# Kernel tuning notes

Hardware: AMD Instinct MI355X
Metric: run time of the kernel (lower is better)

## Reference

```python
import jax, jax.numpy as jnp
import numpy as np

B, L = 2, 1024
D_MODEL = 1024
D_STATE = 16
K = 3            # conv kernel (odd so padding=(K-1)//2 preserves L)
EXPAND = 1       # module is only shape-consistent with d_inner == d_model
D_INNER = D_MODEL * EXPAND


def setup_inputs() -> dict:
    key = jax.random.key(0)
    ks = jax.random.split(key, 10)
    s = 0.02
    x = jax.random.normal(ks[0], (B, L, D_MODEL), dtype=jnp.float32)
    W_in = jax.random.normal(ks[1], (D_MODEL, 2 * D_INNER), dtype=jnp.float32) * s
    conv_w = jax.random.normal(ks[2], (D_INNER, 1, K), dtype=jnp.float32) * s  # depthwise OIH
    W_B = jax.random.normal(ks[3], (D_INNER, D_STATE), dtype=jnp.float32) * s
    W_C = jax.random.normal(ks[4], (D_INNER, D_STATE), dtype=jnp.float32) * s
    W_delta = jax.random.normal(ks[5], (D_INNER, D_MODEL), dtype=jnp.float32) * s
    delta_base = jax.random.normal(ks[6], (D_MODEL,), dtype=jnp.float32)
    W_tau = jax.random.normal(ks[7], (D_MODEL, D_MODEL), dtype=jnp.float32) * s
    A_log = jnp.tile(jnp.log(jnp.arange(1, D_STATE + 1, dtype=jnp.float32)), (D_MODEL, 1))
    W_out = jax.random.normal(ks[8], (D_INNER, D_MODEL), dtype=jnp.float32) * s
    return {"x": x, "W_in": W_in, "conv_w": conv_w, "W_B": W_B, "W_C": W_C,
            "W_delta": W_delta, "delta_base": delta_base, "W_tau": W_tau,
            "A_log": A_log, "W_out": W_out}


def _silu(v):
    return v * jax.nn.sigmoid(v)


def _mamba_fwd(x, W_in, conv_w, W_B, W_C, W_delta, delta_base, W_tau, A_log, W_out):
    residual = x
    z = x @ W_in                               # [B,L,2*D_INNER]
    val, gate = jnp.split(z, 2, axis=-1)
    # depthwise causal-ish conv1d (padding=(K-1)//2)
    v = jnp.transpose(val, (0, 2, 1))          # [B,C,L]
    v = jax.lax.conv_general_dilated(
        v, conv_w, window_strides=(1,), padding=[((K - 1) // 2, (K - 1) // 2)],
        dimension_numbers=("NCH", "OIH", "NCH"), feature_group_count=D_INNER)
    val = jnp.transpose(_silu(v), (0, 2, 1))   # [B,L,D_INNER]

    B_proj = val @ W_B                          # [B,L,N]
    C_proj = val @ W_C                          # [B,L,N]
    combined_delta = val @ W_delta + delta_base # [B,L,D_MODEL]
    Delta = jax.nn.softplus(combined_delta @ W_tau)  # [B,L,D]

    A = -jnp.exp(A_log)                         # [D,N]
    dA = Delta[..., None] * A                   # [B,L,D,N]
    A_bar = jnp.exp(dA)
    B_bar = jnp.expm1(dA) / (dA + 1e-6) * Delta[..., None] * B_proj[:, :, None, :]

    def step(h, inp):
        a_t, b_t, c_t, u_t = inp                # a/b:[B,D,N], c:[B,N], u:[B,D]
        h = a_t * h + b_t * u_t[..., None]
        y_t = jnp.sum(h * c_t[:, None, :], axis=-1)  # [B,D]
        return h, y_t

    h0 = jnp.zeros((x.shape[0], D_INNER, D_STATE), dtype=x.dtype)
    xs = (jnp.moveaxis(A_bar, 1, 0), jnp.moveaxis(B_bar, 1, 0),
          jnp.moveaxis(C_proj, 1, 0), jnp.moveaxis(val, 1, 0))
    _, ys = jax.lax.scan(step, h0, xs)          # ys: [L,B,D]
    y = jnp.moveaxis(ys, 0, 1)                  # [B,L,D]

    out = (y * _silu(gate)) @ W_out + residual  # [B,L,D_MODEL]
    return out


def reference(x, W_in, conv_w, W_B, W_C, W_delta, delta_base, W_tau, A_log, W_out):
    return _mamba_fwd(x, W_in, conv_w, W_B, W_C, W_delta, delta_base, W_tau, A_log, W_out)
```

## Files before the change

kernel.cpp:

```cpp
#include <hip/hip_runtime.h>
#include <math.h>

#define BB 2
#define LL 1024
#define DM 1024
#define DI 1024
#define DS 16
#define ROWS (BB * LL)
#define CH 16
#define NCH (LL / CH)
#define NP 1152
#define NF 1152

typedef unsigned short ushort_t;
typedef __attribute__((ext_vector_type(8))) short short8;
typedef __attribute__((ext_vector_type(4))) float f32x4;
typedef __attribute__((ext_vector_type(4))) float f4;
typedef __attribute__((ext_vector_type(4))) ushort_t us4;

static __device__ __forceinline__ float sp_f(float x) {
    return fmaxf(x, 0.f) + log1pf(expf(-fabsf(x)));
}
static __device__ __forceinline__ ushort_t f2bf(float f) {
    unsigned u = __float_as_uint(f);
    u += 0x7fffu + ((u >> 16) & 1u);
    return (ushort_t)(u >> 16);
}
static __device__ __forceinline__ float bf2f(ushort_t s) {
    return __uint_as_float(((unsigned)s) << 16);
}

#define SWZ(L) ((L) ^ ((((L) >> 7) & 7) << 4))

static __device__ __forceinline__ void gl_lds16(const void* g, void* l) {
    __builtin_amdgcn_global_load_lds(
        (const __attribute__((address_space(1))) unsigned int*)g,
        (__attribute__((address_space(3))) unsigned int*)l, 16, 0, 0);
}

template <int ACT, bool HAS_BIAS, bool HAS_RES, bool OUTBF, int PROJMODE>
__global__ __launch_bounds__(256) void gemm_bf_k(
    const ushort_t* __restrict__ A, const ushort_t* __restrict__ Bt,
    const float* __restrict__ bias, const float* __restrict__ res,
    void* __restrict__ Cout, float* __restrict__ BpO, float* __restrict__ CpO,
    int M, int N, int K, int ldc)
{
    __shared__ __align__(16) char lsa[2][8192];
    __shared__ __align__(16) char lsb[2][16384];

    const int tid = threadIdx.x;
    const int lane = tid & 63;
    const int w = tid >> 6;
    const int wr = w >> 1, wc = w & 1;

    int wg = blockIdx.y * gridDim.x + blockIdx.x;
    const int nwg = gridDim.x * gridDim.y;
    wg = (wg & 7) * (nwg >> 3) + (wg >> 3);
    const int bx = wg % gridDim.x, by = wg / gridDim.x;
    const int row0 = by * 64, col0 = bx * 128;

    const int rl = lane & 15, q = lane >> 4;

    const char* gA[2];
#pragma unroll
    for (int j = 0; j < 2; ++j) {
        int L = SWZ((w * 2 + j) * 1024 + lane * 16);
        gA[j] = (const char*)A + ((size_t)(row0 + (L >> 7)) * K) * 2 + (L & 127);
    }
    const char* gB[4];
#pragma unroll
    for (int j = 0; j < 4; ++j) {
        int L = SWZ((w * 4 + j) * 1024 + lane * 16);
        gB[j] = (const char*)Bt + ((size_t)(col0 + (L >> 7)) * K) * 2 + (L & 127);
    }

    int LA[2][2], LB[4][2];
#pragma unroll
    for (int m = 0; m < 2; ++m)
#pragma unroll
        for (int kk = 0; kk < 2; ++kk)
            LA[m][kk] = SWZ((wr * 32 + m * 16 + rl) * 128 + kk * 64 + q * 16);
#pragma unroll
    for (int n = 0; n < 4; ++n)
#pragma unroll
        for (int kk = 0; kk < 2; ++kk)
            LB[n][kk] = SWZ((wc * 64 + n * 16 + rl) * 128 + kk * 64 + q * 16);

    f32x4 acc[2][4] = {};
    const int NT = K >> 6;

#pragma unroll
    for (int j = 0; j < 2; ++j) gl_lds16(gA[j], &lsa[0][(w * 2 + j) * 1024]);
#pragma unroll
    for (int j = 0; j < 4; ++j) gl_lds16(gB[j], &lsb[0][(w * 4 + j) * 1024]);

    int cur = 0;
    for (int kt = 0; kt < NT; ++kt) {
        if (kt + 1 < NT) {
            const int kb = (kt + 1) * 128;
#pragma unroll
            for (int j = 0; j < 2; ++j)
                gl_lds16(gA[j] + kb, &lsa[cur ^ 1][(w * 2 + j) * 1024]);
#pragma unroll
            for (int j = 0; j < 4; ++j)
                gl_lds16(gB[j] + kb, &lsb[cur ^ 1][(w * 4 + j) * 1024]);
            asm volatile("s_waitcnt vmcnt(6)\n\ts_barrier" ::: "memory");
        } else {
            asm volatile("s_waitcnt vmcnt(0)\n\ts_barrier" ::: "memory");
        }
        short8 af[2][2], bfr[4][2];
#pragma unroll
        for (int m = 0; m < 2; ++m)
#pragma unroll
            for (int kk = 0; kk < 2; ++kk)
                af[m][kk] = *(const short8*)(&lsa[cur][LA[m][kk]]);
#pragma unroll
        for (int n = 0; n < 4; ++n)
#pragma unroll
            for (int kk = 0; kk < 2; ++kk)
                bfr[n][kk] = *(const short8*)(&lsb[cur][LB[n][kk]]);
#pragma unroll
        for (int kk = 0; kk < 2; ++kk)
#pragma unroll
            for (int m = 0; m < 2; ++m)
#pragma unroll
                for (int n = 0; n < 4; ++n)
                    acc[m][n] = __builtin_amdgcn_mfma_f32_16x16x32_bf16(
                        af[m][kk], bfr[n][kk], acc[m][n], 0, 0, 0);
        asm volatile("s_barrier" ::: "memory");
        cur ^= 1;
    }

    float bia[4];
#pragma unroll
    for (int n = 0; n < 4; ++n) {
        int c = col0 + wc * 64 + n * 16 + rl;
        bia[n] = (HAS_BIAS && c < DM) ? bias[c] : 0.f;
    }
#pragma unroll
    for (int m = 0; m < 2; ++m) {
#pragma unroll
        for (int n = 0; n < 4; ++n) {
            int c = col0 + wc * 64 + n * 16 + rl;
#pragma unroll
            for (int i = 0; i < 4; ++i) {
                int r = row0 + wr * 32 + m * 16 + q * 4 + i;
                float v = acc[m][n][i];
                if (PROJMODE == 1 && c >= DM) {
                    if (c < DM + DS)          BpO[(size_t)r * DS + (c - DM)] = v;
                    else if (c < DM + 2 * DS) CpO[(size_t)r * DS + (c - DM - DS)] = v;
                } else if (PROJMODE == 2 && c >= DM) {
                    if (c == DM) BpO[r] = v;
                } else {
                    v += bia[n];
                    if (ACT == 1) v = sp_f(v);
                    if (HAS_RES) v += res[(size_t)r * ldc + c];
                    if (OUTBF) ((ushort_t*)Cout)[(size_t)r * ldc + c] = f2bf(v);
                    else       ((float*)Cout)[(size_t)r * ldc + c] = v;
                }
            }
        }
    }
}

static __device__ __forceinline__ void tconv_body(
    const float* __restrict__ in, ushort_t* __restrict__ out,
    int K, int N, int n0, int k0, float (*t)[33], int tid)
{
    int lx = tid & 31, ly = tid >> 5;
#pragma unroll
    for (int i = 0; i < 32; i += 8)
        t[ly + i][lx] = in[(size_t)(k0 + ly + i) * N + n0 + lx];
    __syncthreads();
#pragma unroll
    for (int i = 0; i < 32; i += 8)
        out[(size_t)(n0 + ly + i) * K + k0 + lx] = f2bf(t[lx][ly + i]);
}

__global__ __launch_bounds__(256) void prep_k(
    const float* __restrict__ x, const float* __restrict__ W_in,
    const float* __restrict__ W_B, const float* __restrict__ W_C,
    const float* __restrict__ W_delta, const float* __restrict__ db,
    const float* __restrict__ W_tau, const float* __restrict__ W_out,
    ushort_t* __restrict__ x_bf, ushort_t* __restrict__ WinT,
    ushort_t* __restrict__ WtT, ushort_t* __restrict__ WoT,
    ushort_t* __restrict__ WdX, ushort_t* __restrict__ WdcT)
{
    __shared__ float t[32][33];
    const int blk = blockIdx.x;
    const int tid = threadIdx.x;
    if (blk < 2048) {
        int i = blk * 256 + tid;
        f4 v = ((const f4*)x)[i];
        us4 o; o.x = f2bf(v.x); o.y = f2bf(v.y); o.z = f2bf(v.z); o.w = f2bf(v.w);
        ((us4*)x_bf)[i] = o;
    } else if (blk < 3072) {
        int i = (blk - 2048) * 256 + tid;
        f4 v = ((const f4*)W_delta)[i];
        us4 o; o.x = f2bf(v.x); o.y = f2bf(v.y); o.z = f2bf(v.z); o.w = f2bf(v.w);
        ((us4*)WdX)[i] = o;
    } else if (blk < 3584) {
        int i = (blk - 3072) * 256 + tid;
        int k = i & 1023, r = i >> 10;
        WdX[(size_t)(1024 + r) * 1024 + k] = (r == 0) ? f2bf(db[k]) : (ushort_t)0;
    } else if (blk < 5632) {
        int tau = blk - 3584;
        tconv_body(W_in, WinT, 1024, 2048, (tau & 63) * 32, (tau >> 6) * 32, t, tid);
    } else if (blk < 6656) {
        int tau = blk - 5632;
        tconv_body(W_tau, WtT, 1024, 1024, (tau & 31) * 32, (tau >> 5) * 32, t, tid);
    } else if (blk < 7680) {
        int tau = blk - 6656;
        tconv_body(W_out, WoT, 1024, 1024, (tau & 31) * 32, (tau >> 5) * 32, t, tid);
    } else {
        int i = (blk - 7680) * 256 + tid;
        int k = i & 1023, r = i >> 10;
        ushort_t v = 0;
        if (r < DS)          v = f2bf(W_B[(size_t)k * DS + r]);
        else if (r < 2 * DS) v = f2bf(W_C[(size_t)k * DS + (r - DS)]);
        WdcT[(size_t)(1024 + r) * 1024 + k] = v;
    }
}

__global__ __launch_bounds__(256) void conv_silu_k(
    const ushort_t* __restrict__ z_bf, const float* __restrict__ cw,
    ushort_t* __restrict__ val_bf)
{
    int t = blockIdx.x * 256 + threadIdx.x;
    int c0 = (t & 255) * 4;
    int row = t >> 8;
    int l = row & (LL - 1);
    const ushort_t* zr = z_bf + (size_t)row * (2 * DI) + c0;
    us4 zz = {0, 0, 0, 0};
    us4 vm = (l > 0)      ? *(const us4*)(zr - 2 * DI) : zz;
    us4 v0 = *(const us4*)(zr);
    us4 vp = (l < LL - 1) ? *(const us4*)(zr + 2 * DI) : zz;
    const f4* wp = (const f4*)(cw + (size_t)c0 * 3);
    f4 w0 = wp[0], w1 = wp[1], w2 = wp[2];
    float w[12];
#pragma unroll
    for (int k = 0; k < 4; ++k) { w[k] = w0[k]; w[4 + k] = w1[k]; w[8 + k] = w2[k]; }
    us4 o;
#pragma unroll
    for (int j = 0; j < 4; ++j) {
        float s = bf2f(vm[j]) * w[3 * j] + bf2f(v0[j]) * w[3 * j + 1]
                + bf2f(vp[j]) * w[3 * j + 2];
        float si = s / (1.f + __expf(-s));
        o[j] = f2bf(si);
    }
    *(us4*)(val_bf + (size_t)row * DI + c0) = o;
}

__global__ __launch_bounds__(256) void scan_p1_k(
    const ushort_t* __restrict__ Del_bf, const ushort_t* __restrict__ val_bf,
    const float* __restrict__ Bp, const float* __restrict__ A_log,
    float* __restrict__ aprod, float* __restrict__ hloc)
{
    int t = blockIdx.x * 256 + threadIdx.x;
    int d = t & (DI - 1);
    int c = (t >> 10) & (NCH - 1);
    int b = t >> 16;

    float Adn[DS], ci[DS];
    const f4* alp = (const f4*)(A_log + (size_t)d * DS);
#pragma unroll
    for (int j = 0; j < 4; ++j) {
        f4 al = alp[j];
#pragma unroll
        for (int k = 0; k < 4; ++k) {
            float a = -__expf(al[k]);
            Adn[j * 4 + k] = a;
            ci[j * 4 + k] = 1.0f / a;
        }
    }
    int row0 = b * LL + c * CH;
    const ushort_t* Dp = Del_bf + (size_t)row0 * DI + d;
    const ushort_t* up = val_bf + (size_t)row0 * DI + d;
    const f4* bp = (const f4*)(Bp + (size_t)row0 * DS);

    float h[DS];
#pragma unroll
    for (int n = 0; n < DS; ++n) h[n] = 0.f;
    float sdv = 0.f;

#pragma unroll 2
    for (int l = 0; l < CH; ++l) {
        float dv = bf2f(Dp[(size_t)l * DI]);
        float u  = bf2f(up[(size_t)l * DI]);
        f4 q0 = bp[l * 4 + 0], q1 = bp[l * 4 + 1], q2 = bp[l * 4 + 2], q3 = bp[l * 4 + 3];
        float bn[DS];
#pragma unroll
        for (int k = 0; k < 4; ++k) {
            bn[k] = q0[k]; bn[4 + k] = q1[k]; bn[8 + k] = q2[k]; bn[12 + k] = q3[k];
        }
        sdv += dv;
#pragma unroll
        for (int n = 0; n < DS; ++n) {
            float a  = __expf(dv * Adn[n]);
            float tt = (ci[n] * bn[n]) * u;
            float s  = h[n] + tt;
            h[n] = fmaf(a, s, -tt);
        }
    }
    size_t o = (((size_t)b * NCH + c) * DI + d) * DS;
#pragma unroll
    for (int j = 0; j < 4; ++j) {
        f4 hv, av;
#pragma unroll
        for (int k = 0; k < 4; ++k) {
            hv[k] = h[j * 4 + k];
            av[k] = __expf(sdv * Adn[j * 4 + k]);
        }
        *(f4*)(hloc + o + j * 4) = hv;
        *(f4*)(aprod + o + j * 4) = av;
    }
}

__global__ __launch_bounds__(256) void scan_p2_k(
    const float* __restrict__ aprod, const float* __restrict__ hloc,
    float* __restrict__ hin)
{
    int t = blockIdx.x * 256 + threadIdx.x;
    int dn = t & (DI * DS - 1);
    int b = t >> 14;
    float h = 0.f;
    size_t base = (size_t)b * NCH * DI * DS + dn;
#pragma unroll 4
    for (int c = 0; c < NCH; ++c) {
        size_t idx = base + (size_t)c * (DI * DS);
        hin[idx] = h;
        h = fmaf(aprod[idx], h, hloc[idx]);
    }
}

__global__ __launch_bounds__(256) void scan_p3_k(
    const ushort_t* __restrict__ Del_bf, const ushort_t* __restrict__ val_bf,
    const float* __restrict__ Bp, const float* __restrict__ Cp,
    const float* __restrict__ A_log, const float* __restrict__ hin,
    const ushort_t* __restrict__ z_bf, ushort_t* __restrict__ g_bf)
{
    int t = blockIdx.x * 256 + threadIdx.x;
    int d = t & (DI - 1);
    int c = (t >> 10) & (NCH - 1);
    int b = t >> 16;

    float Adn[DS], ci[DS];
    const f4* alp = (const f4*)(A_log + (size_t)d * DS);
#pragma unroll
    for (int j = 0; j < 4; ++j) {
        f4 al = alp[j];
#pragma unroll
        for (int k = 0; k < 4; ++k) {
            float a = -__expf(al[k]);
            Adn[j * 4 + k] = a;
            ci[j * 4 + k] = 1.0f / a;
        }
    }
    int row0 = b * LL + c * CH;
    const ushort_t* Dp = Del_bf + (size_t)row0 * DI + d;
    const ushort_t* up = val_bf + (size_t)row0 * DI + d;
    const ushort_t* zp = z_bf + (size_t)row0 * (2 * DI) + DI + d;
    const f4* bp = (const f4*)(Bp + (size_t)row0 * DS);
    const f4* cp = (const f4*)(Cp + (size_t)row0 * DS);
    ushort_t* gp = g_bf + (size_t)row0 * DI + d;

    float h[DS];
    size_t o = (((size_t)b * NCH + c) * DI + d) * DS;
#pragma unroll
    for (int j = 0; j < 4; ++j) {
        f4 hv = *(const f4*)(hin + o + j * 4);
#pragma unroll
        for (int k = 0; k < 4; ++k) h[j * 4 + k] = hv[k];
    }

#pragma unroll 2
    for (int l = 0; l < CH; ++l) {
        float dv = bf2f(Dp[(size_t)l * DI]);
        float u  = bf2f(up[(size_t)l * DI]);
        f4 q0 = bp[l * 4 + 0], q1 = bp[l * 4 + 1], q2 = bp[l * 4 + 2], q3 = bp[l * 4 + 3];
        f4 r0 = cp[l * 4 + 0], r1 = cp[l * 4 + 1], r2 = cp[l * 4 + 2], r3 = cp[l * 4 + 3];
        float bn[DS], cn[DS];
#pragma unroll
        for (int k = 0; k < 4; ++k) {
            bn[k] = q0[k]; bn[4 + k] = q1[k]; bn[8 + k] = q2[k]; bn[12 + k] = q3[k];
            cn[k] = r0[k]; cn[4 + k] = r1[k]; cn[8 + k] = r2[k]; cn[12 + k] = r3[k];
        }
        float psum = 0.f;
#pragma unroll
        for (int n = 0; n < DS; ++n) {
            float a  = __expf(dv * Adn[n]);
            float tt = (ci[n] * bn[n]) * u;
            float s  = h[n] + tt;
            h[n] = fmaf(a, s, -tt);
            psum = fmaf(h[n], cn[n], psum);
        }
        float zg = bf2f(zp[(size_t)l * 2 * DI]);
        float si = zg / (1.f + __expf(-zg));
        gp[(size_t)l * DI] = f2bf(psum * si);
    }
}

extern "C" void kernel_launch(void* const* d_in, const int* in_sizes, int n_in,
                              void* d_out, int out_size, void* d_ws, size_t ws_size,
                              hipStream_t stream)
{
    (void)in_sizes; (void)n_in; (void)out_size; (void)ws_size;

    const float* x        = (const float*)d_in[0];
    const float* W_in     = (const float*)d_in[1];
    const float* conv_w   = (const float*)d_in[2];
    const float* W_B      = (const float*)d_in[3];
    const float* W_C      = (const float*)d_in[4];
    const float* W_delta  = (const float*)d_in[5];
    const float* delta_b  = (const float*)d_in[6];
    const float* W_tau    = (const float*)d_in[7];
    const float* A_log    = (const float*)d_in[8];
    const float* W_out    = (const float*)d_in[9];
    float* out = (float*)d_out;

    const size_t M1 = 1024 * 1024;
    ushort_t* us = (ushort_t*)d_ws;
    ushort_t* z_bf   = us;
    ushort_t* val_bf = us + 4 * M1;
    ushort_t* Del_bf = us + 6 * M1;
    ushort_t* x_bf   = us + 8 * M1;
    ushort_t* g_bf   = us + 10 * M1;
    ushort_t* WinT   = us + 12 * M1;
    ushort_t* WoT    = us + 14 * M1;
    ushort_t* WtT    = us + 15 * M1;
    ushort_t* WdX    = us + 16 * M1;
    ushort_t* WdcT   = WdX + (size_t)NF * 1024;
    float* fb    = (float*)(us + 20 * M1);
    float* Bp    = fb;
    float* Cp    = fb + (size_t)ROWS * DS;
    float* b2    = fb + 2 * (size_t)ROWS * DS;
    float* aprod = b2 + 1024;
    float* hloc  = aprod + 2 * M1;
    float* hin   = hloc + 2 * M1;

    prep_k<<<8192, 256, 0, stream>>>(x, W_in, W_B, W_C, W_delta, delta_b,
                                     W_tau, W_out, x_bf, WinT, WtT, WoT, WdX, WdcT);

    gemm_bf_k<0, false, false, true, 2><<<dim3(NF / 128, DM / 64), 256, 0, stream>>>(
        WtT, WdX, nullptr, nullptr, WdcT, b2, nullptr, DM, NF, DM, DM);

    gemm_bf_k<0, false, false, true, 0><<<dim3(2 * DI / 128, ROWS / 64), 256, 0, stream>>>(
        x_bf, WinT, nullptr, nullptr, z_bf, nullptr, nullptr, ROWS, 2 * DI, DM, 2 * DI);

    conv_silu_k<<<(ROWS * DI / 4) / 256, 256, 0, stream>>>(z_bf, conv_w, val_bf);

    gemm_bf_k<1, true, false, true, 1><<<dim3(NP / 128, ROWS / 64), 256, 0, stream>>>(
        val_bf, WdcT, b2, nullptr, Del_bf, Bp, Cp, ROWS, NP, DI, DM);

    scan_p1_k<<<(BB * NCH * DI) / 256, 256, 0, stream>>>(
        Del_bf, val_bf, Bp, A_log, aprod, hloc);
    scan_p2_k<<<(BB * DI * DS) / 256, 256, 0, stream>>>(aprod, hloc, hin);
    scan_p3_k<<<(BB * NCH * DI) / 256, 256, 0, stream>>>(
        Del_bf, val_bf, Bp, Cp, A_log, hin, z_bf, g_bf);

    gemm_bf_k<0, false, true, false, 0><<<dim3(DM / 128, ROWS / 64), 256, 0, stream>>>(
        g_bf, WoT, nullptr, x, out, nullptr, nullptr, ROWS, DM, DI, DM);
}
```

Baseline: 231.2 us.

## Fuse three-pass chunked scan into one kernel with LDS carry propagation

Replaces the three scan kernels (local chunk scan, global carry pass, rescan) with a single kernel. Each block handles 4 channels across all 64 chunks and keeps per-chunk decay products and local states in shared memory, with swizzled slots to limit bank conflicts. The carry is propagated serially by 64 threads before the rescan. This removes the global aprod/hloc/hin round trips and two launches, at the cost of a serial 64-step LDS phase in which most threads sit idle, and coalescing of Del/val loads across only 4 adjacent channels.

New measurement: 220.4 us. 1.05x faster.

```diff
diff --git a/kernel.cpp b/kernel.cpp
--- a/kernel.cpp
+++ b/kernel.cpp
@@ -251,15 +251,23 @@
     *(us4*)(val_bf + (size_t)row * DI + c0) = o;
 }
 
-__global__ __launch_bounds__(256) void scan_p1_k(
+static __device__ __forceinline__ int slot4(int t, int j) {
+    return t * 64 + 16 * (j ^ ((t >> 1) & 3));
+}
+
+__global__ __launch_bounds__(256) void scan_f_k(
     const ushort_t* __restrict__ Del_bf, const ushort_t* __restrict__ val_bf,
-    const float* __restrict__ Bp, const float* __restrict__ A_log,
-    float* __restrict__ aprod, float* __restrict__ hloc)
-{
-    int t = blockIdx.x * 256 + threadIdx.x;
-    int d = t & (DI - 1);
-    int c = (t >> 10) & (NCH - 1);
-    int b = t >> 16;
+    const float* __restrict__ Bp, const float* __restrict__ Cp,
+    const float* __restrict__ A_log, const ushort_t* __restrict__ z_bf,
+    ushort_t* __restrict__ g_bf)
+{
+    __shared__ __align__(16) char lap[16384];
+    __shared__ __align__(16) char lhl[16384];
+
+    const int tid = threadIdx.x;
+    const int d_sub = tid & 3, c = tid >> 2;
+    const int b = blockIdx.x >> 8;
+    const int d = (blockIdx.x & 255) * 4 + d_sub;
 
     float Adn[DS], ci[DS];
     const f4* alp = (const f4*)(A_log + (size_t)d * DS);
@@ -273,16 +281,18 @@
             ci[j * 4 + k] = 1.0f / a;
         }
     }
-    int row0 = b * LL + c * CH;
+    const int row0 = b * LL + c * CH;
     const ushort_t* Dp = Del_bf + (size_t)row0 * DI + d;
     const ushort_t* up = val_bf + (size_t)row0 * DI + d;
+    const ushort_t* zp = z_bf + (size_t)row0 * (2 * DI) + DI + d;
     const f4* bp = (const f4*)(Bp + (size_t)row0 * DS);
+    const f4* cp = (const f4*)(Cp + (size_t)row0 * DS);
+    ushort_t* gp = g_bf + (size_t)row0 * DI + d;
 
     float h[DS];
 #pragma unroll
     for (int n = 0; n < DS; ++n) h[n] = 0.f;
     float sdv = 0.f;
-
 #pragma unroll 2
     for (int l = 0; l < CH; ++l) {
         float dv = bf2f(Dp[(size_t)l * DI]);
@@ -302,7 +312,6 @@
             h[n] = fmaf(a, s, -tt);
         }
     }
-    size_t o = (((size_t)b * NCH + c) * DI + d) * DS;
 #pragma unroll
     for (int j = 0; j < 4; ++j) {
         f4 hv, av;
@@ -311,68 +320,32 @@
             hv[k] = h[j * 4 + k];
             av[k] = __expf(sdv * Adn[j * 4 + k]);
         }
-        *(f4*)(hloc + o + j * 4) = hv;
-        *(f4*)(aprod + o + j * 4) = av;
-    }
-}
-
-__global__ __launch_bounds__(256) void scan_p2_k(
-    const float* __restrict__ aprod, const float* __restrict__ hloc,
-    float* __restrict__ hin)
-{
-    int t = blockIdx.x * 256 + threadIdx.x;
-    int dn = t & (DI * DS - 1);
-    int b = t >> 14;
-    float h = 0.f;
-    size_t base = (size_t)b * NCH * DI * DS + dn;
-#pragma unroll 4
-    for (int c = 0; c < NCH; ++c) {
-        size_t idx = base + (size_t)c * (DI * DS);
-        hin[idx] = h;
-        h = fmaf(aprod[idx], h, hloc[idx]);
-    }
-}
-
-__global__ __launch_bounds__(256) void scan_p3_k(
-    const ushort_t* __restrict__ Del_bf, const ushort_t* __restrict__ val_bf,
-    const float* __restrict__ Bp, const float* __restrict__ Cp,
-    const float* __restrict__ A_log, const float* __restrict__ hin,
-    const ushort_t* __restrict__ z_bf, ushort_t* __restrict__ g_bf)
-{
-    int t = blockIdx.x * 256 + threadIdx.x;
-    int d = t & (DI - 1);
-    int c = (t >> 10) & (NCH - 1);
-    int b = t >> 16;
-
-    float Adn[DS], ci[DS];
-    const f4* alp = (const f4*)(A_log + (size_t)d * DS);
+        *(f4*)(lap + slot4(tid, j)) = av;
+        *(f4*)(lhl + slot4(tid, j)) = hv;
+    }
+    __syncthreads();
+
+    if (tid < 64) {
+        int ds2 = tid >> 4, n = tid & 15;
+        int jj = n >> 2, ee = 4 * (n & 3);
+        float h2 = 0.f;
+#pragma unroll 8
+        for (int c2 = 0; c2 < NCH; ++c2) {
+            int off = slot4(c2 * 4 + ds2, jj) + ee;
+            float ap = *(const float*)(lap + off);
+            float hl = *(const float*)(lhl + off);
+            *(float*)(lap + off) = h2;
+            h2 = fmaf(ap, h2, hl);
+        }
+    }
+    __syncthreads();
+
 #pragma unroll
     for (int j = 0; j < 4; ++j) {
-        f4 al = alp[j];
-#pragma unroll
-        for (int k = 0; k < 4; ++k) {
-            float a = -__expf(al[k]);
-            Adn[j * 4 + k] = a;
-            ci[j * 4 + k] = 1.0f / a;
-        }
-    }
-    int row0 = b * LL + c * CH;
-    const ushort_t* Dp = Del_bf + (size_t)row0 * DI + d;
-    const ushort_t* up = val_bf + (size_t)row0 * DI + d;
-    const ushort_t* zp = z_bf + (size_t)row0 * (2 * DI) + DI + d;
-    const f4* bp = (const f4*)(Bp + (size_t)row0 * DS);
-    const f4* cp = (const f4*)(Cp + (size_t)row0 * DS);
-    ushort_t* gp = g_bf + (size_t)row0 * DI + d;
-
-    float h[DS];
-    size_t o = (((size_t)b * NCH + c) * DI + d) * DS;
-#pragma unroll
-    for (int j = 0; j < 4; ++j) {
-        f4 hv = *(const f4*)(hin + o + j * 4);
+        f4 hv = *(const f4*)(lap + slot4(tid, j));
 #pragma unroll
         for (int k = 0; k < 4; ++k) h[j * 4 + k] = hv[k];
     }
-
 #pragma unroll 2
     for (int l = 0; l < CH; ++l) {
         float dv = bf2f(Dp[(size_t)l * DI]);
@@ -434,9 +407,6 @@
     float* Bp    = fb;
     float* Cp    = fb + (size_t)ROWS * DS;
     float* b2    = fb + 2 * (size_t)ROWS * DS;
-    float* aprod = b2 + 1024;
-    float* hloc  = aprod + 2 * M1;
-    float* hin   = hloc + 2 * M1;
 
     prep_k<<<8192, 256, 0, stream>>>(x, W_in, W_B, W_C, W_delta, delta_b,
                                      W_tau, W_out, x_bf, WinT, WtT, WoT, WdX, WdcT);
@@ -452,11 +422,8 @@
     gemm_bf_k<1, true, false, true, 1><<<dim3(NP / 128, ROWS / 64), 256, 0, stream>>>(
         val_bf, WdcT, b2, nullptr, Del_bf, Bp, Cp, ROWS, NP, DI, DM);
 
-    scan_p1_k<<<(BB * NCH * DI) / 256, 256, 0, stream>>>(
-        Del_bf, val_bf, Bp, A_log, aprod, hloc);
-    scan_p2_k<<<(BB * DI * DS) / 256, 256, 0, stream>>>(aprod, hloc, hin);
-    scan_p3_k<<<(BB * NCH * DI) / 256, 256, 0, stream>>>(
-        Del_bf, val_bf, Bp, Cp, A_log, hin, z_bf, g_bf);
+    scan_f_k<<<BB * (DI / 4), 256, 0, stream>>>(
+        Del_bf, val_bf, Bp, Cp, A_log, z_bf, g_bf);
 
     gemm_bf_k<0, false, true, false, 0><<<dim3(DM / 128, ROWS / 64), 256, 0, stream>>>(
         g_bf, WoT, nullptr, x, out, nullptr, nullptr, ROWS, DM, DI, DM);
```
